# Performance work log

Hardware: AMD Instinct MI355X
Metric: run time of the kernel (lower is better)

Reference implementation:

```python
import jax, jax.numpy as jnp
import numpy as np

WS = 4        # window_size
SHIFT = 3     # shift_size
HEADS = 4
DIM = 128
HR, WR = 256, 256  # input_resolution (matches post-upsample H, W)


def _rel_pos_index(ws):
    coords = np.stack(np.meshgrid(np.arange(ws), np.arange(ws), indexing='ij'))  # (2, ws, ws)
    cf = coords.reshape(2, -1)
    rel = (cf[:, :, None] - cf[:, None, :]).transpose(1, 2, 0).astype(np.int64)
    rel[:, :, 0] += ws - 1
    rel[:, :, 1] += ws - 1
    rel[:, :, 0] *= 2 * ws - 1
    return rel.sum(-1)  # (N, N)


def _attn_mask(H, W, ws, shift):
    img = np.zeros((H, W))
    cnt = 0
    sl = (slice(0, -ws), slice(-ws, -shift), slice(-shift, None))
    for hs in sl:
        for wsl in sl:
            img[hs, wsl] = cnt
            cnt += 1
    mw = img.reshape(H // ws, ws, W // ws, ws).transpose(0, 2, 1, 3).reshape(-1, ws * ws)
    diff = mw[:, None, :] - mw[:, :, None]  # unsqueeze(1) - unsqueeze(2)
    return np.where(diff != 0, -100.0, 0.0).astype(np.float32)  # (nW, N, N)


REL_IDX = jnp.asarray(_rel_pos_index(WS))
ATTN_MASK = jnp.asarray(_attn_mask(HR, WR, WS, SHIFT))


def _upsample2x_ac(x):
    def interp(x, axis):
        n = x.shape[axis]
        m = 2 * n
        pos = jnp.arange(m) * ((n - 1) / (m - 1))
        lo = jnp.floor(pos).astype(jnp.int32)
        hi = jnp.minimum(lo + 1, n - 1)
        w = (pos - lo).astype(x.dtype)
        shp = [1] * x.ndim
        shp[axis] = m
        w = w.reshape(shp)
        return jnp.take(x, lo, axis=axis) * (1 - w) + jnp.take(x, hi, axis=axis) * w
    return interp(interp(x, 2), 3)


def _conv2d(x, w, b, pad):
    y = jax.lax.conv_general_dilated(x, w, (1, 1), [(pad, pad), (pad, pad)],
                                     dimension_numbers=('NCHW', 'OIHW', 'NCHW'))
    return y + b[None, :, None, None]


def _bn(x, g, b, m, v):
    # eval-mode BatchNorm2d
    s = g / jnp.sqrt(v + 1e-5)
    return x * s[None, :, None, None] + (b - m * s)[None, :, None, None]


def setup_inputs():
    key = jax.random.key(0)
    ks = jax.random.split(key, 8)
    f = jax.random.normal
    return {
        'x': f(ks[0], (4, 256, 128, 64), jnp.float32),
        'qkv_w': f(ks[1], (DIM, 3 * DIM), jnp.float32) * 0.02,
        'qkv_b': jnp.zeros((3 * DIM,), jnp.float32),
        'proj_w': f(ks[2], (DIM, DIM), jnp.float32) * 0.02,
        'proj_b': jnp.zeros((DIM,), jnp.float32),
        'rpb': f(ks[3], ((2 * WS - 1) ** 2, HEADS), jnp.float32) * 0.02,
        'conv1_w': f(ks[4], (256, 256, 3, 3), jnp.float32) * 0.02,
        'conv1_b': jnp.zeros((256,), jnp.float32),
        'bn1_g': jnp.ones((256,), jnp.float32),
        'bn1_b': jnp.zeros((256,), jnp.float32),
        'bn1_m': jnp.zeros((256,), jnp.float32),
        'bn1_v': jnp.ones((256,), jnp.float32),
        'conv2_w': f(ks[5], (256, 256, 3, 3), jnp.float32) * 0.02,
        'conv2_b': jnp.zeros((256,), jnp.float32),
        'bn2_g': jnp.ones((256,), jnp.float32),
        'bn2_b': jnp.zeros((256,), jnp.float32),
        'bn2_m': jnp.zeros((256,), jnp.float32),
        'bn2_v': jnp.ones((256,), jnp.float32),
        'idc_w': f(ks[6], (256, 256, 1, 1), jnp.float32) * 0.02,
        'idc_b': jnp.zeros((256,), jnp.float32),
        'bni_g': jnp.ones((256,), jnp.float32),
        'bni_b': jnp.zeros((256,), jnp.float32),
        'bni_m': jnp.zeros((256,), jnp.float32),
        'bni_v': jnp.ones((256,), jnp.float32),
    }


def reference(x, qkv_w, qkv_b, proj_w, proj_b, rpb,
              conv1_w, conv1_b, bn1_g, bn1_b, bn1_m, bn1_v,
              conv2_w, conv2_b, bn2_g, bn2_b, bn2_m, bn2_v,
              idc_w, idc_b, bni_g, bni_b, bni_m, bni_v):
    x = _upsample2x_ac(x)                 # (B, 256, 256, 128), treated as (B,H,W,C) downstream
    B, H, W, C = x.shape
    shortcut = x
    xs = jnp.roll(x, (-SHIFT, -SHIFT), axis=(1, 2))
    # window partition -> (B*nW, N, C)
    nWh, nWw = H // WS, W // WS
    xw = xs.reshape(B, nWh, WS, nWw, WS, C).transpose(0, 1, 3, 2, 4, 5).reshape(-1, WS * WS, C)
    B_, N, _ = xw.shape
    hd = C // HEADS
    qkv = (xw @ qkv_w + qkv_b).reshape(B_, N, 3, HEADS, hd).transpose(2, 0, 3, 1, 4)
    q, k, v = qkv[0], qkv[1], qkv[2]
    attn = jnp.einsum('bhnd,bhmd->bhnm', q * (hd ** -0.5), k)
    bias = rpb[REL_IDX.reshape(-1)].reshape(N, N, HEADS).transpose(2, 0, 1)  # (h, N, N)
    attn = attn + bias[None]
    nW = ATTN_MASK.shape[0]
    attn = attn.reshape(B_ // nW, nW, HEADS, N, N) + ATTN_MASK[None, :, None]
    attn = jax.nn.softmax(attn.reshape(B_, HEADS, N, N), axis=-1)
    out = jnp.einsum('bhnm,bhmd->bhnd', attn, v).transpose(0, 2, 1, 3).reshape(B_, N, C)
    out = out @ proj_w + proj_b
    # window reverse + roll back
    out = out.reshape(B, nWh, nWw, WS, WS, C).transpose(0, 1, 3, 2, 4, 5).reshape(B, H, W, C)
    out = jnp.roll(out, (SHIFT, SHIFT), axis=(1, 2))
    x = shortcut + out
    # DoubleConv with identity branch (tensor treated as NCHW, per original code)
    y = _conv2d(x, conv1_w, conv1_b, 1)
    y = jax.nn.relu(_bn(y, bn1_g, bn1_b, bn1_m, bn1_v))
    y = _conv2d(y, conv2_w, conv2_b, 1)
    y = _bn(y, bn2_g, bn2_b, bn2_m, bn2_v)
    idn = _bn(_conv2d(x, idc_w, idc_b, 0), bni_g, bni_b, bni_m, bni_v)
    return jax.nn.relu(y + idn)
```

## Files before the change

### kernel.cpp

```cpp
#include <hip/hip_runtime.h>
#include <hip/hip_bf16.h>
#include <math.h>
#include <cstddef>

#define BATCH 4
#define WDIM 256
#define CDIM 128
#define WS 4
#define SHIFT 3
#define HEADS 4
#define HD 32
#define NTOK 16

typedef __attribute__((ext_vector_type(8))) short short8;
typedef __attribute__((ext_vector_type(4))) int int4v;
typedef __attribute__((ext_vector_type(4))) float f32x4;

__device__ __forceinline__ int regionOf(int v) {
    return v < (WDIM - WS) ? 0 : (v < (WDIM - SHIFT) ? 1 : 2);
}

__device__ __forceinline__ short f2bf(float v) {
    __hip_bfloat16 h = __float2bfloat16(v);
    return __builtin_bit_cast(short, h);
}
__device__ __forceinline__ float bf2f(short s) {
    unsigned u = ((unsigned)(unsigned short)s) << 16;
    return __builtin_bit_cast(float, u);
}

__global__ __launch_bounds__(256) void repack_attnw(
    const float* __restrict__ qkv_w,
    const float* __restrict__ proj_w,
    __hip_bfloat16* __restrict__ qkvw_rep,
    __hip_bfloat16* __restrict__ projw_rep)
{
    int idx = blockIdx.x * 256 + threadIdx.x;
    if (idx < 49152) {
        int j = idx >> 7, c = idx & 127;
        qkvw_rep[idx] = __float2bfloat16(qkv_w[c * 384 + j]);
    } else {
        int k = idx - 49152;
        int j = k >> 7, c = k & 127;
        projw_rep[k] = __float2bfloat16(proj_w[c * 128 + j]);
    }
}

__global__ __launch_bounds__(256, 4) void attn_kernel(
    const float* __restrict__ xin,
    const __hip_bfloat16* __restrict__ qkvw_rep,
    const __hip_bfloat16* __restrict__ projw_rep,
    const float* __restrict__ qkv_b,
    const float* __restrict__ proj_b,
    const float* __restrict__ rpb,
    __hip_bfloat16* __restrict__ xatt)
{
    __shared__ __align__(16) char smem[40848];
    float* xrowF  = (float*)smem;
    short* qkvs   = (short*)smem;
    short* aoutS  = (short*)smem;
    short* Xb     = (short*)(smem + 16896);
    short* Ps     = (short*)(smem + 25600);
    short* Vt     = (short*)(smem + 29696);
    float* rpbs   = (float*)(smem + 37888);
    float* qkvbS  = (float*)(smem + 38672);
    float* projbS = (float*)(smem + 40208);
    float* tokw2  = (float*)(smem + 40720);

    const int tid = threadIdx.x;
    const int bid = blockIdx.x;
    const int l   = tid & 63;
    const int wv  = tid >> 6;
    const int lm  = l & 15;
    const int lq  = l >> 4;

    if (tid < 196) rpbs[tid] = rpb[tid];
    for (int i = tid; i < 384; i += 256) qkvbS[i] = qkv_b[i];
    if (tid < 128) projbS[tid] = proj_b[tid];

    #pragma unroll
    for (int k = 0; k < 4; k++) {
        int id = tid + k * 256;
        int n   = id >> 5;
        int row = (id >> 4) & 1;
        int ll  = id & 15;
        int w_  = n >> 4, nn = n & 15;
        int win = bid * 2 + w_;
        int b   = win >> 12;
        int wh  = (win >> 6) & 63;
        int ww  = win & 63;
        int r = nn >> 2, c = nn & 3;
        int gh = (wh * 4 + r + SHIFT) & 255;
        int gw = (ww * 4 + c + SHIFT) & 255;
        float pos2 = gw * (127.0f / 255.0f);
        int lo2 = (int)floorf(pos2);
        int hi2 = min(lo2 + 1, 127);
        if (row == 0 && ll == 0) tokw2[n] = pos2 - (float)lo2;
        int src = row == 0 ? lo2 : hi2;
        const float4* rp = (const float4*)(xin + (((size_t)b * 256 + gh) * 128 + src) * 64);
        ((float4*)(xrowF + n * 132 + row * 64))[ll] = rp[ll];
    }
    __syncthreads();

    {
        int n = tid >> 3;
        int jj = tid & 7;
        float w2 = tokw2[n];
        const float* xr0 = xrowF + n * 132;
        const float* xr1 = xr0 + 64;
        #pragma unroll
        for (int i = 0; i < 16; i++) {
            int cc = jj * 16 + i;
            float pos3 = cc * (63.0f / 127.0f);
            int lo3 = (int)floorf(pos3);
            int hi3 = min(lo3 + 1, 63);
            float w3 = pos3 - (float)lo3;
            float v0 = xr0[lo3] * (1.f - w3) + xr0[hi3] * w3;
            float v1 = xr1[lo3] * (1.f - w3) + xr1[hi3] * w3;
            Xb[n * 136 + cc] = f2bf(v0 * (1.f - w2) + v1 * w2);
        }
    }
    __syncthreads();

    {
        f32x4 qacc[6][2];
        #pragma unroll
        for (int a = 0; a < 6; a++)
            #pragma unroll
            for (int t = 0; t < 2; t++) qacc[a][t] = (f32x4)0.0f;

        for (int ks = 0; ks < 4; ks++) {
            short8 af[6];
            #pragma unroll
            for (int jj = 0; jj < 6; jj++) {
                const int4v* gp = (const int4v*)(qkvw_rep +
                    (size_t)(wv * 96 + jj * 16 + lm) * 128 + ks * 32 + lq * 8);
                af[jj] = __builtin_bit_cast(short8, *gp);
            }
            short8 bfr[2];
            #pragma unroll
            for (int tt = 0; tt < 2; tt++)
                bfr[tt] = *(const short8*)&Xb[(tt * 16 + lm) * 136 + ks * 32 + lq * 8];
            #pragma unroll
            for (int jj = 0; jj < 6; jj++)
                #pragma unroll
                for (int tt = 0; tt < 2; tt++)
                    qacc[jj][tt] = __builtin_amdgcn_mfma_f32_16x16x32_bf16(
                        af[jj], bfr[tt], qacc[jj][tt], 0, 0, 0);
        }
        #pragma unroll
        for (int jj = 0; jj < 6; jj++) {
            int jbase = wv * 96 + jj * 16 + lq * 4;
            #pragma unroll
            for (int tt = 0; tt < 2; tt++) {
                int tok = tt * 16 + lm;
                if (jbase < 128) {
                    float v0 = (qacc[jj][tt][0] + qkvbS[jbase+0]) * 0.17677669529663687f;
                    float v1 = (qacc[jj][tt][1] + qkvbS[jbase+1]) * 0.17677669529663687f;
                    float v2 = (qacc[jj][tt][2] + qkvbS[jbase+2]) * 0.17677669529663687f;
                    float v3 = (qacc[jj][tt][3] + qkvbS[jbase+3]) * 0.17677669529663687f;
                    unsigned p0 = (unsigned short)f2bf(v0) | ((unsigned)(unsigned short)f2bf(v1) << 16);
                    unsigned p1 = (unsigned short)f2bf(v2) | ((unsigned)(unsigned short)f2bf(v3) << 16);
                    *(unsigned*)&qkvs[tok * 264 + jbase]     = p0;
                    *(unsigned*)&qkvs[tok * 264 + jbase + 2] = p1;
                } else if (jbase < 256) {
                    float v0 = qacc[jj][tt][0] + qkvbS[jbase+0];
                    float v1 = qacc[jj][tt][1] + qkvbS[jbase+1];
                    float v2 = qacc[jj][tt][2] + qkvbS[jbase+2];
                    float v3 = qacc[jj][tt][3] + qkvbS[jbase+3];
                    unsigned p0 = (unsigned short)f2bf(v0) | ((unsigned)(unsigned short)f2bf(v1) << 16);
                    unsigned p1 = (unsigned short)f2bf(v2) | ((unsigned)(unsigned short)f2bf(v3) << 16);
                    *(unsigned*)&qkvs[tok * 264 + jbase]     = p0;
                    *(unsigned*)&qkvs[tok * 264 + jbase + 2] = p1;
                } else {
                    #pragma unroll
                    for (int r = 0; r < 4; r++) {
                        int d = jbase - 256 + r;
                        Vt[(tt * 128 + d) * 16 + lm] = f2bf(qacc[jj][tt][r] + qkvbS[jbase + r]);
                    }
                }
            }
        }
    }
    __syncthreads();

    {
        int w_ = wv >> 1;
        int hb = (wv & 1) * 2;
        int win = bid * 2 + w_;
        int wh = (win >> 6) & 63;
        int ww = win & 63;
        int m  = lm;
        int r2 = m >> 2, c2 = m & 3;
        int reg2 = regionOf(wh * 4 + r2) * 3 + regionOf(ww * 4 + c2);
        #pragma unroll
        for (int hh = 0; hh < 2; hh++) {
            int h = hb + hh;
            short8 qa = *(const short8*)&qkvs[(w_ * 16 + lm) * 264 + h * 32 + lq * 8];
            short8 kb = *(const short8*)&qkvs[(w_ * 16 + lm) * 264 + 128 + h * 32 + lq * 8];
            f32x4 s = __builtin_amdgcn_mfma_f32_16x16x32_bf16(qa, kb, (f32x4)0.0f, 0, 0, 0);
            #pragma unroll
            for (int r = 0; r < 4; r++) {
                int n = lq * 4 + r;
                int r1 = n >> 2, c1 = n & 3;
                int ridx = (r1 - r2 + 3) * 7 + (c1 - c2 + 3);
                float v = s[r] + rpbs[ridx * 4 + h];
                int reg1 = regionOf(wh * 4 + r1) * 3 + regionOf(ww * 4 + c1);
                if (reg1 != reg2) v -= 100.f;
                float mx = v;
                mx = fmaxf(mx, __shfl_xor(mx, 1));
                mx = fmaxf(mx, __shfl_xor(mx, 2));
                mx = fmaxf(mx, __shfl_xor(mx, 4));
                mx = fmaxf(mx, __shfl_xor(mx, 8));
                float e = __expf(v - mx);
                float ss = e;
                ss += __shfl_xor(ss, 1);
                ss += __shfl_xor(ss, 2);
                ss += __shfl_xor(ss, 4);
                ss += __shfl_xor(ss, 8);
                Ps[((w_ * 4 + h) * 16 + n) * 16 + m] = f2bf(e / ss);
            }
        }
    }
    __syncthreads();

    {
        int w_ = wv >> 1;
        int hb = (wv & 1) * 2;
        #pragma unroll
        for (int hh = 0; hh < 2; hh++) {
            int h = hb + hh;
            #pragma unroll
            for (int dt = 0; dt < 2; dt++) {
                short8 pa = (short8)0;
                short8 vb = (short8)0;
                if (lq < 2) {
                    pa = *(const short8*)&Ps[((w_ * 4 + h) * 16 + lm) * 16 + lq * 8];
                    vb = *(const short8*)&Vt[(w_ * 128 + h * 32 + dt * 16 + lm) * 16 + lq * 8];
                }
                f32x4 o = __builtin_amdgcn_mfma_f32_16x16x32_bf16(pa, vb, (f32x4)0.0f, 0, 0, 0);
                #pragma unroll
                for (int r = 0; r < 4; r++) {
                    aoutS[(w_ * 16 + lq * 4 + r) * 136 + h * 32 + dt * 16 + lm] = f2bf(o[r]);
                }
            }
        }
    }
    __syncthreads();

    {
        f32x4 cacc[2][2];
        #pragma unroll
        for (int a = 0; a < 2; a++)
            #pragma unroll
            for (int t = 0; t < 2; t++) cacc[a][t] = (f32x4)0.0f;

        for (int ks = 0; ks < 4; ks++) {
            short8 af[2];
            #pragma unroll
            for (int jj = 0; jj < 2; jj++) {
                const int4v* gp = (const int4v*)(projw_rep +
                    (size_t)(wv * 32 + jj * 16 + lm) * 128 + ks * 32 + lq * 8);
                af[jj] = __builtin_bit_cast(short8, *gp);
            }
            short8 bfr[2];
            #pragma unroll
            for (int tt = 0; tt < 2; tt++)
                bfr[tt] = *(const short8*)&aoutS[(tt * 16 + lm) * 136 + ks * 32 + lq * 8];
            #pragma unroll
            for (int jj = 0; jj < 2; jj++)
                #pragma unroll
                for (int tt = 0; tt < 2; tt++)
                    cacc[jj][tt] = __builtin_amdgcn_mfma_f32_16x16x32_bf16(
                        af[jj], bfr[tt], cacc[jj][tt], 0, 0, 0);
        }
        __syncthreads();
        #pragma unroll
        for (int jj = 0; jj < 2; jj++) {
            int jbase = wv * 32 + jj * 16 + lq * 4;
            #pragma unroll
            for (int tt = 0; tt < 2; tt++) {
                int tok = tt * 16 + lm;
                float v0 = cacc[jj][tt][0] + projbS[jbase+0] + bf2f(Xb[tok * 136 + jbase+0]);
                float v1 = cacc[jj][tt][1] + projbS[jbase+1] + bf2f(Xb[tok * 136 + jbase+1]);
                float v2 = cacc[jj][tt][2] + projbS[jbase+2] + bf2f(Xb[tok * 136 + jbase+2]);
                float v3 = cacc[jj][tt][3] + projbS[jbase+3] + bf2f(Xb[tok * 136 + jbase+3]);
                unsigned p0 = (unsigned short)f2bf(v0) | ((unsigned)(unsigned short)f2bf(v1) << 16);
                unsigned p1 = (unsigned short)f2bf(v2) | ((unsigned)(unsigned short)f2bf(v3) << 16);
                *(unsigned*)&aoutS[tok * 136 + jbase]     = p0;
                *(unsigned*)&aoutS[tok * 136 + jbase + 2] = p1;
            }
        }
    }
    __syncthreads();

    {
        #pragma unroll
        for (int k = 0; k < 4; k++) {
            int idx = k * 256 + tid;
            int j  = idx & 127;
            int c  = (idx >> 7) & 3;
            int w_ = idx >> 9;
            int win = bid * 2 + w_;
            int b   = win >> 12;
            int wh  = (win >> 6) & 63;
            int ww  = win & 63;
            int gw  = (ww * 4 + c + SHIFT) & 255;
            int slot0 = (wh * 4 + SHIFT + 1) & 255;
            unsigned short s0 = (unsigned short)aoutS[(w_ * 16 + 0 + c) * 136 + j];
            unsigned short s1 = (unsigned short)aoutS[(w_ * 16 + 4 + c) * 136 + j];
            unsigned short s2 = (unsigned short)aoutS[(w_ * 16 + 8 + c) * 136 + j];
            unsigned short s3 = (unsigned short)aoutS[(w_ * 16 + 12 + c) * 136 + j];
            unsigned long long pk =
                (unsigned long long)s0 | ((unsigned long long)s1 << 16) |
                ((unsigned long long)s2 << 32) | ((unsigned long long)s3 << 48);
            size_t base = (((size_t)b * 256 + gw) * 128 + j) * 256 + slot0;
            *(unsigned long long*)(xatt + base) = pk;
        }
    }
}

__global__ __launch_bounds__(256) void repack3(
    const float* __restrict__ w, const float* __restrict__ bias,
    const float* __restrict__ g_, const float* __restrict__ b_,
    const float* __restrict__ m_, const float* __restrict__ v_,
    __hip_bfloat16* __restrict__ wrep, float* __restrict__ cconst, int roll)
{
    int idx = blockIdx.x * 256 + threadIdx.x;
    int co = idx / 2304;
    int rem = idx - co * 2304;
    int ci = rem / 9;
    int tap = rem - ci * 9;
    float s = g_[co] * rsqrtf(v_[co] + 1e-5f);
    int ci_s = (ci + roll) & 255;
    size_t o = ((((size_t)(co >> 7) * 8 + (ci_s >> 5)) * 9 + tap) * 128 + (co & 127)) * 32 + (ci_s & 31);
    wrep[o] = __float2bfloat16(w[idx] * s);
    if (rem == 0) cconst[co] = bias[co] * s + (b_[co] - m_[co] * s);
}

__global__ __launch_bounds__(256) void repack1(
    const float* __restrict__ w, const float* __restrict__ bias,
    const float* __restrict__ g_, const float* __restrict__ b_,
    const float* __restrict__ m_, const float* __restrict__ v_,
    __hip_bfloat16* __restrict__ wrep, float* __restrict__ cconst)
{
    int idx = blockIdx.x * 256 + threadIdx.x;
    int co = idx >> 8, ci = idx & 255;
    float s = g_[co] * rsqrtf(v_[co] + 1e-5f);
    int ci_s = (ci + 1) & 255;
    wrep[(((size_t)(co >> 7) * 8 + (ci_s >> 5)) * 128 + (co & 127)) * 32 + (ci_s & 31)] =
        __float2bfloat16(w[idx] * s);
    if (ci == 0) cconst[co] += bias[co] * s + (b_[co] - m_[co] * s);
}

template<int HAS_IDC, int OUT_BF16>
__global__ __launch_bounds__(256) void conv_mfma(
    const __hip_bfloat16* __restrict__ xin,
    const __hip_bfloat16* __restrict__ xidc,
    const __hip_bfloat16* __restrict__ wrep,
    const __hip_bfloat16* __restrict__ wrepi,
    const float* __restrict__ cconst,
    void* __restrict__ outp)
{
    constexpr int NROWS = HAS_IDC ? 4 : 3;
    constexpr int NPER  = NROWS * 2;
    constexpr int NTAPS = HAS_IDC ? 10 : 9;
    __shared__ __align__(16) short xs[NROWS * 130 * 40];

    const int tid = threadIdx.x;
    const int l  = tid & 63;
    const int wv = tid >> 6;
    const int wave_co = (wv & 1) * 64;
    const int wave_w  = (wv >> 1) * 64;
    const int nb = ((blockIdx.x & 7) << 8) | (blockIdx.x >> 3);
    const int g = nb & 1;
    const int h = (nb >> 1) & 255;
    const int n = nb >> 9;
    const int lq = l >> 4;
    const int lm = l & 15;

    if (tid < 192) {
        int row = tid >> 6;
        int side = (tid >> 5) & 1;
        int ci = tid & 31;
        xs[(row * 130 + (side ? 129 : 0)) * 40 + ci] = 0;
    }

    f32x4 acc[4][4];
    #pragma unroll
    for (int a = 0; a < 4; a++)
        #pragma unroll
        for (int b = 0; b < 4; b++) acc[a][b] = (f32x4)0.0f;

    int4v pre[NPER];
    #pragma unroll
    for (int t = 0; t < NPER; t++) {
        int idx = t * 256 + tid;
        int c8  = idx & 3;
        int w   = (idx >> 2) & 127;
        int row = idx >> 9;
        int4v v = {0, 0, 0, 0};
        if (row < 3) {
            int hh = h - 1 + row;
            if (0 <= hh && hh < 256)
                v = *(const int4v*)(xin + ((((size_t)n * 256 + hh) * 128 + w) << 8) + c8 * 8);
        } else {
            v = *(const int4v*)(xidc + ((((size_t)n * 256 + h) * 128 + w) << 8) + c8 * 8);
        }
        pre[t] = v;
    }

    #pragma unroll 1
    for (int cb = 0; cb < 8; cb++) {
        __syncthreads();
        #pragma unroll
        for (int t = 0; t < NPER; t++) {
            int idx = t * 256 + tid;
            int c8  = idx & 3;
            int w   = (idx >> 2) & 127;
            int row = idx >> 9;
            *(int4v*)&xs[(row * 130 + w + 1) * 40 + c8 * 8] = pre[t];
        }
        __syncthreads();
        if (cb < 7) {
            #pragma unroll
            for (int t = 0; t < NPER; t++) {
                int idx = t * 256 + tid;
                int c8  = idx & 3;
                int w   = (idx >> 2) & 127;
                int row = idx >> 9;
                int4v v = {0, 0, 0, 0};
                if (row < 3) {
                    int hh = h - 1 + row;
                    if (0 <= hh && hh < 256)
                        v = *(const int4v*)(xin + ((((size_t)n * 256 + hh) * 128 + w) << 8)
                                            + (cb + 1) * 32 + c8 * 8);
                } else {
                    v = *(const int4v*)(xidc + ((((size_t)n * 256 + h) * 128 + w) << 8)
                                        + (cb + 1) * 32 + c8 * 8);
                }
                pre[t] = v;
            }
        }

        #pragma unroll 1
        for (int tap = 0; tap < NTAPS; tap++) {
            const __hip_bfloat16* ap;
            const short* bs;
            if (tap < 9) {
                int kh = tap / 3;
                int kw = tap - kh * 3;
                ap = wrep + ((((size_t)(g * 8 + cb) * 9 + tap)) << 12);
                bs = xs + (kh * 130 + wave_w + kw) * 40;
            } else {
                ap = wrepi + (((size_t)(g * 8 + cb)) << 12);
                bs = xs + (3 * 130 + wave_w + 1) * 40;
            }
            short8 afr[4];
            #pragma unroll
            for (int cs = 0; cs < 4; cs++) {
                const int4v* p4 = (const int4v*)(ap + (size_t)(wave_co + cs * 16 + lm) * 32 + lq * 8);
                afr[cs] = __builtin_bit_cast(short8, *p4);
            }
            #pragma unroll
            for (int ws = 0; ws < 4; ws++) {
                short8 bfr = __builtin_bit_cast(short8,
                    *(const int4v*)&bs[(ws * 16 + lm) * 40 + lq * 8]);
                #pragma unroll
                for (int cs = 0; cs < 4; cs++) {
                    acc[cs][ws] = __builtin_amdgcn_mfma_f32_16x16x32_bf16(
                        afr[cs], bfr, acc[cs][ws], 0, 0, 0);
                }
            }
        }
    }

    #pragma unroll
    for (int cs = 0; cs < 4; cs++) {
        int co0 = g * 128 + wave_co + cs * 16 + lq * 4;
        float c0 = cconst[co0 + 0], c1 = cconst[co0 + 1];
        float c2 = cconst[co0 + 2], c3 = cconst[co0 + 3];
        #pragma unroll
        for (int ws = 0; ws < 4; ws++) {
            int w = wave_w + ws * 16 + lm;
            float v0 = fmaxf(acc[cs][ws][0] + c0, 0.f);
            float v1 = fmaxf(acc[cs][ws][1] + c1, 0.f);
            float v2 = fmaxf(acc[cs][ws][2] + c2, 0.f);
            float v3 = fmaxf(acc[cs][ws][3] + c3, 0.f);
            if (OUT_BF16) {
                unsigned long long pk =
                    (unsigned long long)(unsigned short)f2bf(v0) |
                    ((unsigned long long)(unsigned short)f2bf(v1) << 16) |
                    ((unsigned long long)(unsigned short)f2bf(v2) << 32) |
                    ((unsigned long long)(unsigned short)f2bf(v3) << 48);
                size_t base = ((((size_t)n * 256 + h) * 128 + w) << 8) + co0;
                *(unsigned long long*)((__hip_bfloat16*)outp + base) = pk;
            } else {
                float* op = (float*)outp;
                op[(((size_t)n * 256 + co0 + 0) * 256 + h) * 128 + w] = v0;
                op[(((size_t)n * 256 + co0 + 1) * 256 + h) * 128 + w] = v1;
                op[(((size_t)n * 256 + co0 + 2) * 256 + h) * 128 + w] = v2;
                op[(((size_t)n * 256 + co0 + 3) * 256 + h) * 128 + w] = v3;
            }
        }
    }
}

extern "C" void kernel_launch(void* const* d_in, const int* in_sizes, int n_in,
                              void* d_out, int out_size, void* d_ws, size_t ws_size,
                              hipStream_t stream) {
    const float* x       = (const float*)d_in[0];
    const float* qkv_w   = (const float*)d_in[1];
    const float* qkv_b   = (const float*)d_in[2];
    const float* proj_w  = (const float*)d_in[3];
    const float* proj_b  = (const float*)d_in[4];
    const float* rpb     = (const float*)d_in[5];
    const float* conv1_w = (const float*)d_in[6];
    const float* conv1_b = (const float*)d_in[7];
    const float* bn1_g   = (const float*)d_in[8];
    const float* bn1_b   = (const float*)d_in[9];
    const float* bn1_m   = (const float*)d_in[10];
    const float* bn1_v   = (const float*)d_in[11];
    const float* conv2_w = (const float*)d_in[12];
    const float* conv2_b = (const float*)d_in[13];
    const float* bn2_g   = (const float*)d_in[14];
    const float* bn2_b   = (const float*)d_in[15];
    const float* bn2_m   = (const float*)d_in[16];
    const float* bn2_v   = (const float*)d_in[17];
    const float* idc_w   = (const float*)d_in[18];
    const float* idc_b   = (const float*)d_in[19];
    const float* bni_g   = (const float*)d_in[20];
    const float* bni_b   = (const float*)d_in[21];
    const float* bni_m   = (const float*)d_in[22];
    const float* bni_v   = (const float*)d_in[23];

    const size_t TE = (size_t)BATCH * 256 * 256 * 128;
    char* ws = (char*)d_ws;
    __hip_bfloat16* xatt  = (__hip_bfloat16*)(ws);
    __hip_bfloat16* y1    = (__hip_bfloat16*)(ws + TE * 2);
    __hip_bfloat16* wrep1 = (__hip_bfloat16*)(ws + TE * 4);
    __hip_bfloat16* wrep2 = (__hip_bfloat16*)(ws + TE * 4 + 1179648);
    __hip_bfloat16* wrepi = (__hip_bfloat16*)(ws + TE * 4 + 2359296);
    float*          c1    = (float*)(ws + TE * 4 + 2490368);
    float*          c2    = (float*)(ws + TE * 4 + 2491392);
    __hip_bfloat16* qkvw_rep = (__hip_bfloat16*)(ws + TE * 4 + 2492416);
    __hip_bfloat16* projw_rep= (__hip_bfloat16*)(ws + TE * 4 + 2590720);

    repack3<<<2304, 256, 0, stream>>>(conv1_w, conv1_b, bn1_g, bn1_b, bn1_m, bn1_v, wrep1, c1, 1);
    repack3<<<2304, 256, 0, stream>>>(conv2_w, conv2_b, bn2_g, bn2_b, bn2_m, bn2_v, wrep2, c2, 0);
    repack1<<<256, 256, 0, stream>>>(idc_w, idc_b, bni_g, bni_b, bni_m, bni_v, wrepi, c2);
    repack_attnw<<<256, 256, 0, stream>>>(qkv_w, proj_w, qkvw_rep, projw_rep);

    attn_kernel<<<8192, 256, 0, stream>>>(x, qkvw_rep, projw_rep, qkv_b, proj_b, rpb, xatt);

    conv_mfma<0, 1><<<2048, 256, 0, stream>>>(xatt, nullptr, wrep1, nullptr, c1, (void*)y1);
    conv_mfma<1, 0><<<2048, 256, 0, stream>>>(y1, xatt, wrep2, wrepi, c2, d_out);
}
```

Before: 721.1 us.

## Double-buffer conv weight fragments, transpose attention softmax, and pad upsample staging layout

In the conv kernel, the per-tap weight-fragment loads are double-buffered so the next tap's global loads are issued while the current tap's MFMAs run. The next channel-block activation prefetch is moved later, next to the final taps. In the attention kernel, the QK MFMA operands are swapped so each lane holds four keys of one query row, which replaces four 16-lane shuffle reductions with in-register reductions plus two cross-quad shuffles, and the P output is written as packed 64-bit stores. The upsample staging buffer is transposed to a stride-33 layout to avoid LDS bank conflicts, with packed bf16 stores; the cost is higher register pressure and more complex code.

Result: no change. 719.3 us (-0.3%).

```diff
diff --git a/kernel.cpp b/kernel.cpp
--- a/kernel.cpp
+++ b/kernel.cpp
@@ -46,6 +46,8 @@
     }
 }
 
+#define XROW_RS 2114
+
 __global__ __launch_bounds__(256, 4) void attn_kernel(
     const float* __restrict__ xin,
     const __hip_bfloat16* __restrict__ qkvw_rep,
@@ -55,17 +57,17 @@
     const float* __restrict__ rpb,
     __hip_bfloat16* __restrict__ xatt)
 {
-    __shared__ __align__(16) char smem[40848];
+    __shared__ __align__(16) char smem[40864];
     float* xrowF  = (float*)smem;
     short* qkvs   = (short*)smem;
     short* aoutS  = (short*)smem;
-    short* Xb     = (short*)(smem + 16896);
-    short* Ps     = (short*)(smem + 25600);
-    short* Vt     = (short*)(smem + 29696);
-    float* rpbs   = (float*)(smem + 37888);
-    float* qkvbS  = (float*)(smem + 38672);
-    float* projbS = (float*)(smem + 40208);
-    float* tokw2  = (float*)(smem + 40720);
+    short* Xb     = (short*)(smem + 16912);
+    short* Ps     = (short*)(smem + 25616);
+    short* Vt     = (short*)(smem + 29712);
+    float* rpbs   = (float*)(smem + 37904);
+    float* qkvbS  = (float*)(smem + 38688);
+    float* projbS = (float*)(smem + 40224);
+    float* tokw2  = (float*)(smem + 40736);
 
     const int tid = threadIdx.x;
     const int bid = blockIdx.x;
@@ -98,7 +100,12 @@
         if (row == 0 && ll == 0) tokw2[n] = pos2 - (float)lo2;
         int src = row == 0 ? lo2 : hi2;
         const float4* rp = (const float4*)(xin + (((size_t)b * 256 + gh) * 128 + src) * 64);
-        ((float4*)(xrowF + n * 132 + row * 64))[ll] = rp[ll];
+        float4 v = rp[ll];
+        float* bp = xrowF + row * XROW_RS + n + (4 * ll) * 33;
+        bp[0]      = v.x;
+        bp[33]     = v.y;
+        bp[66]     = v.z;
+        bp[99]     = v.w;
     }
     __syncthreads();
 
@@ -106,18 +113,24 @@
         int n = tid >> 3;
         int jj = tid & 7;
         float w2 = tokw2[n];
-        const float* xr0 = xrowF + n * 132;
-        const float* xr1 = xr0 + 64;
-        #pragma unroll
-        for (int i = 0; i < 16; i++) {
-            int cc = jj * 16 + i;
-            float pos3 = cc * (63.0f / 127.0f);
-            int lo3 = (int)floorf(pos3);
-            int hi3 = min(lo3 + 1, 63);
-            float w3 = pos3 - (float)lo3;
-            float v0 = xr0[lo3] * (1.f - w3) + xr0[hi3] * w3;
-            float v1 = xr1[lo3] * (1.f - w3) + xr1[hi3] * w3;
-            Xb[n * 136 + cc] = f2bf(v0 * (1.f - w2) + v1 * w2);
+        const float* x0 = xrowF + n;
+        const float* x1 = x0 + XROW_RS;
+        #pragma unroll
+        for (int p = 0; p < 8; p++) {
+            unsigned pk = 0;
+            #pragma unroll
+            for (int q = 0; q < 2; q++) {
+                int cc = jj * 16 + p * 2 + q;
+                float pos3 = cc * (63.0f / 127.0f);
+                int lo3 = (int)floorf(pos3);
+                float w3 = pos3 - (float)lo3;
+                int o = lo3 * 33;
+                float v0 = x0[o] * (1.f - w3) + x0[o + 33] * w3;
+                float v1 = x1[o] * (1.f - w3) + x1[o + 33] * w3;
+                float out = v0 * (1.f - w2) + v1 * w2;
+                pk |= ((unsigned)(unsigned short)f2bf(out)) << (16 * q);
+            }
+            *(unsigned*)&Xb[n * 136 + jj * 16 + p * 2] = pk;
         }
     }
     __syncthreads();
@@ -190,36 +203,43 @@
         int win = bid * 2 + w_;
         int wh = (win >> 6) & 63;
         int ww = win & 63;
-        int m  = lm;
-        int r2 = m >> 2, c2 = m & 3;
-        int reg2 = regionOf(wh * 4 + r2) * 3 + regionOf(ww * 4 + c2);
+        int nq = lm;
+        int r1 = nq >> 2, c1 = nq & 3;
+        int reg1 = regionOf(wh * 4 + r1) * 3 + regionOf(ww * 4 + c1);
         #pragma unroll
         for (int hh = 0; hh < 2; hh++) {
             int h = hb + hh;
             short8 qa = *(const short8*)&qkvs[(w_ * 16 + lm) * 264 + h * 32 + lq * 8];
             short8 kb = *(const short8*)&qkvs[(w_ * 16 + lm) * 264 + 128 + h * 32 + lq * 8];
-            f32x4 s = __builtin_amdgcn_mfma_f32_16x16x32_bf16(qa, kb, (f32x4)0.0f, 0, 0, 0);
+            f32x4 s = __builtin_amdgcn_mfma_f32_16x16x32_bf16(kb, qa, (f32x4)0.0f, 0, 0, 0);
+            float v[4];
             #pragma unroll
             for (int r = 0; r < 4; r++) {
-                int n = lq * 4 + r;
-                int r1 = n >> 2, c1 = n & 3;
+                int m = lq * 4 + r;
+                int r2 = m >> 2, c2 = m & 3;
                 int ridx = (r1 - r2 + 3) * 7 + (c1 - c2 + 3);
-                float v = s[r] + rpbs[ridx * 4 + h];
-                int reg1 = regionOf(wh * 4 + r1) * 3 + regionOf(ww * 4 + c1);
-                if (reg1 != reg2) v -= 100.f;
-                float mx = v;
-                mx = fmaxf(mx, __shfl_xor(mx, 1));
-                mx = fmaxf(mx, __shfl_xor(mx, 2));
-                mx = fmaxf(mx, __shfl_xor(mx, 4));
-                mx = fmaxf(mx, __shfl_xor(mx, 8));
-                float e = __expf(v - mx);
-                float ss = e;
-                ss += __shfl_xor(ss, 1);
-                ss += __shfl_xor(ss, 2);
-                ss += __shfl_xor(ss, 4);
-                ss += __shfl_xor(ss, 8);
-                Ps[((w_ * 4 + h) * 16 + n) * 16 + m] = f2bf(e / ss);
-            }
+                v[r] = s[r] + rpbs[ridx * 4 + h];
+                int reg2 = regionOf(wh * 4 + r2) * 3 + regionOf(ww * 4 + c2);
+                if (reg2 != reg1) v[r] -= 100.f;
+            }
+            float mx = fmaxf(fmaxf(v[0], v[1]), fmaxf(v[2], v[3]));
+            mx = fmaxf(mx, __shfl_xor(mx, 16));
+            mx = fmaxf(mx, __shfl_xor(mx, 32));
+            float e0 = __expf(v[0] - mx);
+            float e1 = __expf(v[1] - mx);
+            float e2 = __expf(v[2] - mx);
+            float e3 = __expf(v[3] - mx);
+            float ss = (e0 + e1) + (e2 + e3);
+            ss += __shfl_xor(ss, 16);
+            ss += __shfl_xor(ss, 32);
+            float rinv = 1.0f / ss;
+            unsigned plo = (unsigned short)f2bf(e0 * rinv) |
+                           ((unsigned)(unsigned short)f2bf(e1 * rinv) << 16);
+            unsigned phi = (unsigned short)f2bf(e2 * rinv) |
+                           ((unsigned)(unsigned short)f2bf(e3 * rinv) << 16);
+            unsigned long long pk = (unsigned long long)plo |
+                                    ((unsigned long long)phi << 32);
+            *(unsigned long long*)&Ps[((w_ * 4 + h) * 16 + lm) * 16 + lq * 4] = pk;
         }
     }
     __syncthreads();
@@ -422,56 +442,80 @@
             *(int4v*)&xs[(row * 130 + w + 1) * 40 + c8 * 8] = pre[t];
         }
         __syncthreads();
-        if (cb < 7) {
-            #pragma unroll
-            for (int t = 0; t < NPER; t++) {
-                int idx = t * 256 + tid;
-                int c8  = idx & 3;
-                int w   = (idx >> 2) & 127;
-                int row = idx >> 9;
-                int4v v = {0, 0, 0, 0};
-                if (row < 3) {
-                    int hh = h - 1 + row;
-                    if (0 <= hh && hh < 256)
-                        v = *(const int4v*)(xin + ((((size_t)n * 256 + hh) * 128 + w) << 8)
-                                            + (cb + 1) * 32 + c8 * 8);
-                } else {
-                    v = *(const int4v*)(xidc + ((((size_t)n * 256 + h) * 128 + w) << 8)
-                                        + (cb + 1) * 32 + c8 * 8);
-                }
-                pre[t] = v;
-            }
-        }
-
-        #pragma unroll 1
-        for (int tap = 0; tap < NTAPS; tap++) {
-            const __hip_bfloat16* ap;
+
+        short8 afrA[4], afrB[4];
+        auto loadW = [&](int tap, short8* afr) {
+            const __hip_bfloat16* ap = (!HAS_IDC || tap < 9)
+                ? wrep + ((((size_t)(g * 8 + cb) * 9 + tap)) << 12)
+                : wrepi + (((size_t)(g * 8 + cb)) << 12);
+            #pragma unroll
+            for (int cs = 0; cs < 4; cs++)
+                afr[cs] = __builtin_bit_cast(short8,
+                    *(const int4v*)(ap + (size_t)(wave_co + cs * 16 + lm) * 32 + lq * 8));
+        };
+        auto computeT = [&](int tap, short8* afr) {
             const short* bs;
-            if (tap < 9) {
-                int kh = tap / 3;
-                int kw = tap - kh * 3;
-                ap = wrep + ((((size_t)(g * 8 + cb) * 9 + tap)) << 12);
+            if (HAS_IDC && tap == 9) {
+                bs = xs + (3 * 130 + wave_w + 1) * 40;
+            } else {
+                int kh = tap / 3, kw = tap - kh * 3;
                 bs = xs + (kh * 130 + wave_w + kw) * 40;
-            } else {
-                ap = wrepi + (((size_t)(g * 8 + cb)) << 12);
-                bs = xs + (3 * 130 + wave_w + 1) * 40;
-            }
-            short8 afr[4];
-            #pragma unroll
-            for (int cs = 0; cs < 4; cs++) {
-                const int4v* p4 = (const int4v*)(ap + (size_t)(wave_co + cs * 16 + lm) * 32 + lq * 8);
-                afr[cs] = __builtin_bit_cast(short8, *p4);
             }
             #pragma unroll
             for (int ws = 0; ws < 4; ws++) {
                 short8 bfr = __builtin_bit_cast(short8,
                     *(const int4v*)&bs[(ws * 16 + lm) * 40 + lq * 8]);
                 #pragma unroll
-                for (int cs = 0; cs < 4; cs++) {
+                for (int cs = 0; cs < 4; cs++)
                     acc[cs][ws] = __builtin_amdgcn_mfma_f32_16x16x32_bf16(
                         afr[cs], bfr, acc[cs][ws], 0, 0, 0);
+            }
+        };
+        auto prefetch = [&]() {
+            if (cb < 7) {
+                #pragma unroll
+                for (int t = 0; t < NPER; t++) {
+                    int idx = t * 256 + tid;
+                    int c8  = idx & 3;
+                    int w   = (idx >> 2) & 127;
+                    int row = idx >> 9;
+                    int4v v = {0, 0, 0, 0};
+                    if (row < 3) {
+                        int hh = h - 1 + row;
+                        if (0 <= hh && hh < 256)
+                            v = *(const int4v*)(xin + ((((size_t)n * 256 + hh) * 128 + w) << 8)
+                                                + (cb + 1) * 32 + c8 * 8);
+                    } else {
+                        v = *(const int4v*)(xidc + ((((size_t)n * 256 + h) * 128 + w) << 8)
+                                            + (cb + 1) * 32 + c8 * 8);
+                    }
+                    pre[t] = v;
                 }
             }
+        };
+
+        loadW(0, afrA);
+        loadW(1, afrB);
+        computeT(0, afrA);
+        #pragma unroll 1
+        for (int tap = 1; tap + 3 < NTAPS; tap += 2) {
+            loadW(tap + 1, afrA);
+            computeT(tap, afrB);
+            loadW(tap + 2, afrB);
+            computeT(tap + 1, afrA);
+        }
+        if constexpr (HAS_IDC) {
+            loadW(8, afrA);
+            computeT(7, afrB);
+            loadW(9, afrB);
+            prefetch();
+            computeT(8, afrA);
+            computeT(9, afrB);
+        } else {
+            loadW(8, afrA);
+            prefetch();
+            computeT(7, afrB);
+            computeT(8, afrA);
         }
     }
 
```
